# Kernel optimization log

Hardware: AMD Instinct MI355X
Metric: run time of the kernel (lower is better)

Reference implementation:

```python
import jax, jax.numpy as jnp
import numpy as np

EPS = 1e-09

def setup_inputs() -> dict:
    key = jax.random.key(0)
    k1, k2 = jax.random.split(key)
    N, C = 65536, 1024
    pred = jax.random.normal(k1, (N, C), dtype=jnp.float32)
    target = jax.random.randint(k2, (N,), 0, C, dtype=jnp.int64)
    return {"pred": pred, "target": target}

def reference(pred, target):
    # Faithful to the torch module: softmax over dim=0 (across the batch dim)
    p = jax.nn.softmax(pred, axis=0) + EPS  # epsilon added before BOTH log terms
    C = pred.shape[1]
    tar = jax.nn.one_hot(target, C, dtype=pred.dtype)  # [N, C]
    # per-row BCE with log base 2, mean over classes
    bce = tar * jnp.log2(p) + (1.0 - tar) * jnp.log2(1.0 - p)
    loss = -jnp.mean(bce, axis=1)  # [N]
    return jnp.mean(loss)
```

## Files before the change

### kernel.cpp

```cpp
#include <hip/hip_runtime.h>
#include <math.h>

static constexpr int N = 65536;
static constexpr int C = 1024;
static constexpr float EPS = 1e-9f;


template <int RPB>
__global__ __launch_bounds__(256) void colsum_kernel(
    const float* __restrict__ pred, float* __restrict__ partial,
    int* __restrict__ counter) {
    const int tid = threadIdx.x;
    if (blockIdx.x == 0 && tid == 0) *counter = 0;

    const float4* __restrict__ p4 =
        reinterpret_cast<const float4*>(pred) +
        (size_t)blockIdx.x * RPB * (C / 4) + tid;

    float a0 = 0.f, a1 = 0.f, a2 = 0.f, a3 = 0.f;

    float4 v0 = p4[0 * (C / 4)];
    float4 v1 = p4[1 * (C / 4)];
    float4 v2 = p4[2 * (C / 4)];
    float4 v3 = p4[3 * (C / 4)];
    float4 v4 = p4[4 * (C / 4)];
    float4 v5 = p4[5 * (C / 4)];
    float4 v6 = p4[6 * (C / 4)];
    float4 v7 = p4[7 * (C / 4)];
    p4 += 8 * (C / 4);

#pragma unroll 1
    for (int b = 0; b < RPB / 8 - 1; ++b) {
        float4 w0 = p4[0 * (C / 4)];
        float4 w1 = p4[1 * (C / 4)];
        float4 w2 = p4[2 * (C / 4)];
        float4 w3 = p4[3 * (C / 4)];
        float4 w4 = p4[4 * (C / 4)];
        float4 w5 = p4[5 * (C / 4)];
        float4 w6 = p4[6 * (C / 4)];
        float4 w7 = p4[7 * (C / 4)];
        p4 += 8 * (C / 4);
        __builtin_amdgcn_sched_barrier(0);

        a0 += __expf(v0.x); a1 += __expf(v0.y); a2 += __expf(v0.z); a3 += __expf(v0.w);
        a0 += __expf(v1.x); a1 += __expf(v1.y); a2 += __expf(v1.z); a3 += __expf(v1.w);
        a0 += __expf(v2.x); a1 += __expf(v2.y); a2 += __expf(v2.z); a3 += __expf(v2.w);
        a0 += __expf(v3.x); a1 += __expf(v3.y); a2 += __expf(v3.z); a3 += __expf(v3.w);
        a0 += __expf(v4.x); a1 += __expf(v4.y); a2 += __expf(v4.z); a3 += __expf(v4.w);
        a0 += __expf(v5.x); a1 += __expf(v5.y); a2 += __expf(v5.z); a3 += __expf(v5.w);
        a0 += __expf(v6.x); a1 += __expf(v6.y); a2 += __expf(v6.z); a3 += __expf(v6.w);
        a0 += __expf(v7.x); a1 += __expf(v7.y); a2 += __expf(v7.z); a3 += __expf(v7.w);

        v0 = w0; v1 = w1; v2 = w2; v3 = w3;
        v4 = w4; v5 = w5; v6 = w6; v7 = w7;
    }
    a0 += __expf(v0.x); a1 += __expf(v0.y); a2 += __expf(v0.z); a3 += __expf(v0.w);
    a0 += __expf(v1.x); a1 += __expf(v1.y); a2 += __expf(v1.z); a3 += __expf(v1.w);
    a0 += __expf(v2.x); a1 += __expf(v2.y); a2 += __expf(v2.z); a3 += __expf(v2.w);
    a0 += __expf(v3.x); a1 += __expf(v3.y); a2 += __expf(v3.z); a3 += __expf(v3.w);
    a0 += __expf(v4.x); a1 += __expf(v4.y); a2 += __expf(v4.z); a3 += __expf(v4.w);
    a0 += __expf(v5.x); a1 += __expf(v5.y); a2 += __expf(v5.z); a3 += __expf(v5.w);
    a0 += __expf(v6.x); a1 += __expf(v6.y); a2 += __expf(v6.z); a3 += __expf(v6.w);
    a0 += __expf(v7.x); a1 += __expf(v7.y); a2 += __expf(v7.z); a3 += __expf(v7.w);

    reinterpret_cast<float4*>(partial + (size_t)blockIdx.x * C)[tid] =
        make_float4(a0, a1, a2, a3);
}

__global__ __launch_bounds__(256) void colreduce_kernel(
    const float* __restrict__ partial, float* __restrict__ logS, int RB) {
    const int t  = threadIdx.x;
    const int cp = t & 7;
    const int r0 = t >> 3;
    const int c0 = blockIdx.x * 16;
    const int eighth = RB / 8;

    const float2* __restrict__ p2 =
        reinterpret_cast<const float2*>(partial) + (c0 >> 1) + cp;

    float2 a[8];
#pragma unroll
    for (int j = 0; j < 8; ++j) a[j] = make_float2(0.f, 0.f);
    for (int r = r0; r < eighth; r += 32) {
#pragma unroll
        for (int j = 0; j < 8; ++j) {
            const float2 v = p2[(size_t)(r + j * eighth) * (C / 2)];
            a[j].x += v.x;
            a[j].y += v.y;
        }
    }
    float2 s;
    s.x = ((a[0].x + a[1].x) + (a[2].x + a[3].x)) + ((a[4].x + a[5].x) + (a[6].x + a[7].x));
    s.y = ((a[0].y + a[1].y) + (a[2].y + a[3].y)) + ((a[4].y + a[5].y) + (a[6].y + a[7].y));
#pragma unroll
    for (int off = 8; off <= 32; off <<= 1) {
        s.x += __shfl_xor(s.x, off, 64);
        s.y += __shfl_xor(s.y, off, 64);
    }
    __shared__ float2 wred[4][8];
    if ((t & 63) < 8) wred[t >> 6][cp] = s;
    __syncthreads();
    if (t < 8) {
        const float vx = wred[0][t].x + wred[1][t].x + wred[2][t].x + wred[3][t].x;
        const float vy = wred[0][t].y + wred[1][t].y + wred[2][t].y + wred[3][t].y;
        logS[c0 + 2 * t]     = log2f(vx);
        logS[c0 + 2 * t + 1] = log2f(vy);
    }
}

__global__ __launch_bounds__(256) void target_finalize_kernel(
    const int* __restrict__ tgt, const float* __restrict__ pred,
    const float* __restrict__ logS, float* __restrict__ gArr,
    int* __restrict__ counter, float* __restrict__ out) {
    const int t = threadIdx.x;
    const int n = blockIdx.x * 256 + t;
    const int c = tgt[n];
    const float x = pred[((size_t)n << 10) + c];
    const float LOG2E_F = 1.4426950408889634f;
    float v = LOG2E_F * x - logS[c];
#pragma unroll
    for (int off = 32; off > 0; off >>= 1)
        v += __shfl_down(v, off, 64);
    __shared__ float wsum[4];
    if ((t & 63) == 0) wsum[t >> 6] = v;
    __syncthreads();

    __shared__ int last;
    if (t == 0) {
        gArr[blockIdx.x] = wsum[0] + wsum[1] + wsum[2] + wsum[3];
        __threadfence();
        const int old = __hip_atomic_fetch_add(counter, 1, __ATOMIC_ACQ_REL,
                                               __HIP_MEMORY_SCOPE_AGENT);
        last = (old == (int)gridDim.x - 1) ? 1 : 0;
    }
    __syncthreads();
    if (!last) return;

    float gl = __hip_atomic_load(&gArr[t], __ATOMIC_RELAXED,
                                 __HIP_MEMORY_SCOPE_AGENT);
#pragma unroll
    for (int off = 32; off > 0; off >>= 1)
        gl += __shfl_down(gl, off, 64);
    __shared__ float r1[4];
    if ((t & 63) == 0) r1[t >> 6] = gl;
    __syncthreads();
    if (t == 0) {
        const double LOG2E = 1.4426950408889634;
        const double SumContrib = (double)(r1[0] + r1[1] + r1[2] + r1[3]);
        const double termA = -LOG2E * (double)C * (1.0 + (double)N * (double)EPS);
        const double total = termA + SumContrib;
        out[0] = (float)(-total / ((double)N * (double)C));
    }
}

extern "C" void kernel_launch(void* const* d_in, const int* in_sizes, int n_in,
                              void* d_out, int out_size, void* d_ws, size_t ws_size,
                              hipStream_t stream) {
    const float* pred = (const float*)d_in[0];
    const int*   tgt  = (const int*)d_in[1];
    float* wsf     = (float*)d_ws;
    float* logS    = wsf;
    int*   counter = (int*)(wsf + 1024);
    float* gArr    = wsf + 1088;
    float* partial = wsf + 4096;
    const size_t base_bytes = 4096 * sizeof(float);

    int RB = 2048;
    while (RB > 512 && base_bytes + (size_t)RB * C * sizeof(float) > ws_size)
        RB >>= 1;

    if (RB >= 2048)
        colsum_kernel<32><<<2048, 256, 0, stream>>>(pred, partial, counter);
    else if (RB == 1024)
        colsum_kernel<64><<<1024, 256, 0, stream>>>(pred, partial, counter);
    else
        colsum_kernel<128><<<512, 256, 0, stream>>>(pred, partial, counter);

    colreduce_kernel<<<64, 256, 0, stream>>>(partial, logS, RB);
    target_finalize_kernel<<<256, 256, 0, stream>>>(tgt, pred, logS, gArr,
                                                    counter, (float*)d_out);
}
```

Before: 62.78 us.

## Fuse column reduce and target finalize into one spin-synchronized epilogue kernel

Merges the column-reduction kernel and the target/finalize kernel into a single launch. The first 64 blocks compute log column sums and signal a counter, while all 256 blocks spin-wait on that counter before gathering target logits. The partial-row count drops from 2048 to 1024, and the colsum kernel gets an occupancy hint in its launch bounds. This removes one kernel launch and its gap, at the cost of a grid-wide spin barrier that relies on all 256 blocks being co-resident.

```diff
diff --git a/kernel.cpp b/kernel.cpp
--- a/kernel.cpp
+++ b/kernel.cpp
@@ -7,11 +7,11 @@
 
 
 template <int RPB>
-__global__ __launch_bounds__(256) void colsum_kernel(
+__global__ __launch_bounds__(256, 4) void colsum_kernel(
     const float* __restrict__ pred, float* __restrict__ partial,
-    int* __restrict__ counter) {
+    int* __restrict__ counters) {
     const int tid = threadIdx.x;
-    if (blockIdx.x == 0 && tid == 0) *counter = 0;
+    if (blockIdx.x == 0 && tid == 0) { counters[0] = 0; counters[1] = 0; }
 
     const float4* __restrict__ p4 =
         reinterpret_cast<const float4*>(pred) +
@@ -67,57 +67,73 @@
         make_float4(a0, a1, a2, a3);
 }
 
-__global__ __launch_bounds__(256) void colreduce_kernel(
-    const float* __restrict__ partial, float* __restrict__ logS, int RB) {
-    const int t  = threadIdx.x;
-    const int cp = t & 7;
-    const int r0 = t >> 3;
-    const int c0 = blockIdx.x * 16;
-    const int eighth = RB / 8;
+__global__ __launch_bounds__(256) void epilogue_kernel(
+    const float* __restrict__ partial, const int* __restrict__ tgt,
+    const float* __restrict__ pred, float* __restrict__ logS,
+    int* __restrict__ counters, float* __restrict__ gArr,
+    float* __restrict__ out, int RB) {
+    const int t = threadIdx.x;
 
-    const float2* __restrict__ p2 =
-        reinterpret_cast<const float2*>(partial) + (c0 >> 1) + cp;
+    if (blockIdx.x < 64) {
+        const int cp = t & 7;
+        const int r0 = t >> 3;
+        const int c0 = blockIdx.x * 16;
+        const int eighth = RB / 8;
 
-    float2 a[8];
+        const float2* __restrict__ p2 =
+            reinterpret_cast<const float2*>(partial) + (c0 >> 1) + cp;
+
+        float2 a[8];
 #pragma unroll
-    for (int j = 0; j < 8; ++j) a[j] = make_float2(0.f, 0.f);
-    for (int r = r0; r < eighth; r += 32) {
+        for (int j = 0; j < 8; ++j) a[j] = make_float2(0.f, 0.f);
+        for (int r = r0; r < eighth; r += 32) {
 #pragma unroll
-        for (int j = 0; j < 8; ++j) {
-            const float2 v = p2[(size_t)(r + j * eighth) * (C / 2)];
-            a[j].x += v.x;
-            a[j].y += v.y;
+            for (int j = 0; j < 8; ++j) {
+                const float2 v = p2[(size_t)(r + j * eighth) * (C / 2)];
+                a[j].x += v.x;
+                a[j].y += v.y;
+            }
+        }
+        float2 s;
+        s.x = ((a[0].x + a[1].x) + (a[2].x + a[3].x)) + ((a[4].x + a[5].x) + (a[6].x + a[7].x));
+        s.y = ((a[0].y + a[1].y) + (a[2].y + a[3].y)) + ((a[4].y + a[5].y) + (a[6].y + a[7].y));
+#pragma unroll
+        for (int off = 8; off <= 32; off <<= 1) {
+            s.x += __shfl_xor(s.x, off, 64);
+            s.y += __shfl_xor(s.y, off, 64);
+        }
+        __shared__ float2 wred[4][8];
+        if ((t & 63) < 8) wred[t >> 6][cp] = s;
+        __syncthreads();
+        if (t < 8) {
+            const float vx = wred[0][t].x + wred[1][t].x + wred[2][t].x + wred[3][t].x;
+            const float vy = wred[0][t].y + wred[1][t].y + wred[2][t].y + wred[3][t].y;
+            __hip_atomic_store(&logS[c0 + 2 * t],     log2f(vx),
+                               __ATOMIC_RELEASE, __HIP_MEMORY_SCOPE_AGENT);
+            __hip_atomic_store(&logS[c0 + 2 * t + 1], log2f(vy),
+                               __ATOMIC_RELEASE, __HIP_MEMORY_SCOPE_AGENT);
+        }
+        __syncthreads();
+        if (t == 0) {
+            __threadfence();
+            __hip_atomic_fetch_add(&counters[0], 1, __ATOMIC_ACQ_REL,
+                                   __HIP_MEMORY_SCOPE_AGENT);
         }
     }
-    float2 s;
-    s.x = ((a[0].x + a[1].x) + (a[2].x + a[3].x)) + ((a[4].x + a[5].x) + (a[6].x + a[7].x));
-    s.y = ((a[0].y + a[1].y) + (a[2].y + a[3].y)) + ((a[4].y + a[5].y) + (a[6].y + a[7].y));
-#pragma unroll
-    for (int off = 8; off <= 32; off <<= 1) {
-        s.x += __shfl_xor(s.x, off, 64);
-        s.y += __shfl_xor(s.y, off, 64);
+
+    if (t == 0) {
+        while (__hip_atomic_load(&counters[0], __ATOMIC_ACQUIRE,
+                                 __HIP_MEMORY_SCOPE_AGENT) < 64)
+            __builtin_amdgcn_s_sleep(2);
     }
-    __shared__ float2 wred[4][8];
-    if ((t & 63) < 8) wred[t >> 6][cp] = s;
     __syncthreads();
-    if (t < 8) {
-        const float vx = wred[0][t].x + wred[1][t].x + wred[2][t].x + wred[3][t].x;
-        const float vy = wred[0][t].y + wred[1][t].y + wred[2][t].y + wred[3][t].y;
-        logS[c0 + 2 * t]     = log2f(vx);
-        logS[c0 + 2 * t + 1] = log2f(vy);
-    }
-}
 
-__global__ __launch_bounds__(256) void target_finalize_kernel(
-    const int* __restrict__ tgt, const float* __restrict__ pred,
-    const float* __restrict__ logS, float* __restrict__ gArr,
-    int* __restrict__ counter, float* __restrict__ out) {
-    const int t = threadIdx.x;
     const int n = blockIdx.x * 256 + t;
     const int c = tgt[n];
     const float x = pred[((size_t)n << 10) + c];
-    const float LOG2E_F = 1.4426950408889634f;
-    float v = LOG2E_F * x - logS[c];
+    const float ls = __hip_atomic_load(&logS[c], __ATOMIC_RELAXED,
+                                       __HIP_MEMORY_SCOPE_AGENT);
+    float v = 1.4426950408889634f * x - ls;
 #pragma unroll
     for (int off = 32; off > 0; off >>= 1)
         v += __shfl_down(v, off, 64);
@@ -129,7 +145,7 @@
     if (t == 0) {
         gArr[blockIdx.x] = wsum[0] + wsum[1] + wsum[2] + wsum[3];
         __threadfence();
-        const int old = __hip_atomic_fetch_add(counter, 1, __ATOMIC_ACQ_REL,
+        const int old = __hip_atomic_fetch_add(&counters[1], 1, __ATOMIC_ACQ_REL,
                                                __HIP_MEMORY_SCOPE_AGENT);
         last = (old == (int)gridDim.x - 1) ? 1 : 0;
     }
@@ -158,25 +174,21 @@
                               hipStream_t stream) {
     const float* pred = (const float*)d_in[0];
     const int*   tgt  = (const int*)d_in[1];
-    float* wsf     = (float*)d_ws;
-    float* logS    = wsf;
-    int*   counter = (int*)(wsf + 1024);
-    float* gArr    = wsf + 1088;
-    float* partial = wsf + 4096;
+    float* wsf      = (float*)d_ws;
+    float* logS     = wsf;
+    int*   counters = (int*)(wsf + 1024);
+    float* gArr     = wsf + 1088;
+    float* partial  = wsf + 4096;
     const size_t base_bytes = 4096 * sizeof(float);
 
-    int RB = 2048;
-    while (RB > 512 && base_bytes + (size_t)RB * C * sizeof(float) > ws_size)
-        RB >>= 1;
+    int RB = 1024;
+    if (base_bytes + (size_t)RB * C * sizeof(float) > ws_size) RB = 512;
 
-    if (RB >= 2048)
-        colsum_kernel<32><<<2048, 256, 0, stream>>>(pred, partial, counter);
-    else if (RB == 1024)
-        colsum_kernel<64><<<1024, 256, 0, stream>>>(pred, partial, counter);
+    if (RB == 1024)
+        colsum_kernel<64><<<1024, 256, 0, stream>>>(pred, partial, counters);
     else
-        colsum_kernel<128><<<512, 256, 0, stream>>>(pred, partial, counter);
+        colsum_kernel<128><<<512, 256, 0, stream>>>(pred, partial, counters);
 
-    colreduce_kernel<<<64, 256, 0, stream>>>(partial, logS, RB);
-    target_finalize_kernel<<<256, 256, 0, stream>>>(tgt, pred, logS, gArr,
-                                                    counter, (float*)d_out);
+    epilogue_kernel<<<256, 256, 0, stream>>>(partial, tgt, pred, logS,
+                                             counters, gArr, (float*)d_out, RB);
 }
```

Result: slower. 87.15 us (+38.8%).
